# Kernel optimization log

Hardware: AMD Instinct MI355X
Metric: run time of the kernel (lower is better)

## Reference

```python
import jax, jax.numpy as jnp
import numpy as np
from jax import lax

DN = ('NCHW', 'OIHW', 'NCHW')
EPS = 1e-5


def conv2d(x, w, b, pad):
    y = lax.conv_general_dilated(x, w, (1, 1), [(pad, pad), (pad, pad)], dimension_numbers=DN)
    return y + b[None, :, None, None]


def setup_inputs() -> dict:
    B, C, G, O, H, W = 2, 64, 64, 64, 256, 256
    key = jax.random.key(0)
    ks = jax.random.split(key, 12)
    s = 0.05
    return {
        'input': jax.random.normal(ks[0], (B, C, H, W), jnp.float32),
        'guidance': jax.random.normal(ks[1], (B, G, H, W), jnp.float32),
        # channel-wise kernel-generating network (two 3x3 convs)
        'cw_w1': jax.random.normal(ks[2], (C, C + G, 3, 3), jnp.float32) * s,
        'cw_b1': jnp.zeros((C,), jnp.float32),
        'cw_w2': jax.random.normal(ks[3], (9 * C, C, 3, 3), jnp.float32) * s,
        'cw_b2': jnp.zeros((9 * C,), jnp.float32),
        # depth-wise kernel-generating network (3x3 conv -> GAP -> 1x1 conv)
        'dw_w1': jax.random.normal(ks[4], (C, C + G, 3, 3), jnp.float32) * s,
        'dw_b1': jnp.zeros((C,), jnp.float32),
        'dw_w2': jax.random.normal(ks[5], (C * O, C, 1, 1), jnp.float32) * s,
        'dw_b2': jnp.zeros((C * O,), jnp.float32),
        # BatchNorm affine params
        'bn_gamma': jnp.ones((O,), jnp.float32),
        'bn_beta': jnp.zeros((O,), jnp.float32),
    }


def reference(input, guidance, cw_w1, cw_b1, cw_w2, cw_b2,
              dw_w1, dw_b1, dw_w2, dw_b2, bn_gamma, bn_beta):
    B, C, H, W = input.shape
    kgn_in = jnp.concatenate((input, guidance), axis=1)

    # channel-wise per-pixel 3x3 weights: [B, 9C, H, W]
    cw = conv2d(jax.nn.relu(conv2d(kgn_in, cw_w1, cw_b1, 1)), cw_w2, cw_b2, 1)

    # depth-wise per-sample 1x1 weights: [B, C*O, 1, 1]
    h = jax.nn.relu(conv2d(kgn_in, dw_w1, dw_b1, 1))
    h = jnp.mean(h, axis=(2, 3), keepdims=True)  # AdaptiveAvgPool2d((1,1))
    dw = conv2d(h, dw_w2, dw_b2, 0)
    O = dw.shape[1] // C

    # guided separable conv: spatially-varying depthwise 3x3 then per-sample 1x1
    # patches ordered (C, kh, kw) channel-major -> [B, C, 9, H, W]
    patches = lax.conv_general_dilated_patches(
        input, filter_shape=(3, 3), window_strides=(1, 1), padding='SAME',
        dimension_numbers=DN).reshape(B, C, 9, H, W)
    cw = cw.reshape(B, C, 9, H, W)
    y = jnp.sum(patches * cw, axis=2)  # [B, C, H, W]

    dw = dw.reshape(B, O, C)
    z = jnp.einsum('bchw,boc->bohw', y, dw)  # per-sample 1x1 conv

    # BatchNorm2d (training-mode batch stats) + ReLU
    mu = jnp.mean(z, axis=(0, 2, 3), keepdims=True)
    var = jnp.var(z, axis=(0, 2, 3), keepdims=True)
    zn = (z - mu) * lax.rsqrt(var + EPS)
    out = jax.nn.relu(zn * bn_gamma[None, :, None, None] + bn_beta[None, :, None, None])
    return out
```

## Files before the change

kernel.cpp:

```cpp
#include <hip/hip_runtime.h>

typedef short v8s __attribute__((ext_vector_type(8)));
typedef float v4f __attribute__((ext_vector_type(4)));

__device__ inline unsigned short f2bf(float f) {
    unsigned u = __float_as_uint(f);
    u += 0x7fff + ((u >> 16) & 1);
    return (unsigned short)(u >> 16);
}
__device__ inline float bf2f(unsigned short h) {
    return __uint_as_float(((unsigned)h) << 16);
}

__device__ inline void gload_lds16(const void* g, void* l) {
    __builtin_amdgcn_global_load_lds(
        (const __attribute__((address_space(1))) unsigned*)(unsigned long long)(uintptr_t)g,
        (__attribute__((address_space(3))) unsigned*)(unsigned)(uintptr_t)l, 16, 0, 0);
}

__global__ void transpose_kernel(const float* __restrict__ input, const float* __restrict__ guidance,
                                 char* __restrict__ X0, char* __restrict__ inN)
{
    __shared__ unsigned lds[64 * 66];
    const int tid = threadIdx.x;
    const int b = blockIdx.y;
    const size_t hw0 = (size_t)blockIdx.x * 64;

    for (int it = 0; it < 16; ++it) {
        int p  = it * 4 + (tid >> 6);
        int px = tid & 63;
        size_t hw = hw0 + px;
        int c0 = 2 * p;
        float f0 = (c0 < 64) ? input[((size_t)(b * 64 + c0) << 16) + hw]
                             : guidance[((size_t)(b * 64 + c0 - 64) << 16) + hw];
        float f1 = (c0 + 1 < 64) ? input[((size_t)(b * 64 + c0 + 1) << 16) + hw]
                                 : guidance[((size_t)(b * 64 + c0 - 63) << 16) + hw];
        lds[px * 66 + p] = (unsigned)f2bf(f0) | ((unsigned)f2bf(f1) << 16);
    }
    __syncthreads();

    char* xbase = X0 + (((size_t)b * 65536 + hw0) << 8);
    for (int it = 0; it < 4; ++it) {
        int chunk = it * 256 + tid;
        int px  = chunk >> 4;
        int ofs = (chunk & 15) << 4;
        int u   = (ofs - ((px & 7) << 4)) & 255;
        const unsigned* s = &lds[px * 66 + (u >> 2)];
        *(uint4*)(xbase + px * 256 + ofs) = make_uint4(s[0], s[1], s[2], s[3]);
    }
    char* ibase = inN + (((size_t)b * 65536 + hw0) << 7);
    for (int it = 0; it < 2; ++it) {
        int chunk = it * 256 + tid;
        int px  = chunk >> 3;
        int ofs = (chunk & 7) << 4;
        int u   = (ofs - ((px & 7) << 4)) & 127;
        const unsigned* s = &lds[px * 66 + (u >> 2)];
        *(uint4*)(ibase + px * 128 + ofs) = make_uint4(s[0], s[1], s[2], s[3]);
    }
}

__global__ void prepack_all(const float* __restrict__ cw_w2, const float* __restrict__ cw_w1,
                            const float* __restrict__ dw_w1, char* __restrict__ Bp2,
                            char* __restrict__ Bp1, char* __restrict__ Bpdw)
{
    int bid = blockIdx.x;
    if (bid < 1296) {
        int t = bid * 256 + threadIdx.x;
        int jj = t & 7, lane = (t >> 3) & 63;
        int r2 = t >> 9;
        int ng = r2 % 36, r3 = r2 / 36;
        int ick = r3 & 1, tau = r3 >> 1;
        if (tau >= 9) return;
        int n  = ng * 16 + (lane & 15);
        int ic = ick * 32 + (lane >> 4) * 8 + jj;
        int oc = (n & 63) * 9 + (n >> 6);
        float v = cw_w2[(((size_t)oc * 64 + ic) * 3 + tau / 3) * 3 + tau % 3];
        *(unsigned short*)(Bp2 + (size_t)t * 2) = f2bf(v);
    } else {
        int s = bid - 1296;
        int set = (s >= 288);
        const float* src = set ? dw_w1 : cw_w1;
        char* dst = set ? Bpdw : Bp1;
        int t = (set ? s - 288 : s) * 256 + threadIdx.x;
        int jj = t & 7, lane = (t >> 3) & 63;
        int r2 = t >> 9;
        int ng = r2 & 3, r3 = r2 >> 2;
        int ick = r3 & 3, tau = r3 >> 2;
        if (tau >= 9) return;
        int n  = ng * 16 + (lane & 15);
        int ic = ick * 32 + (lane >> 4) * 8 + jj;
        float v = src[(((size_t)n * 128 + ic) * 3 + tau / 3) * 3 + tau % 3];
        *(unsigned short*)(dst + (size_t)t * 2) = f2bf(v);
    }
}

__global__ __launch_bounds__(256, 3) void conv1_mfma(
    const char* __restrict__ X0, const char* __restrict__ Bp1, const char* __restrict__ Bp2,
    const float* __restrict__ b1, const float* __restrict__ b2,
    char* __restrict__ t1, float* __restrict__ hsum)
{
    constexpr int PP = 66 * 256;
    __shared__ __align__(16) char As[3 * PP];

    const int tid = threadIdx.x, lane = tid & 63, w = tid >> 6;
    const int m16 = lane & 15, q = lane >> 4;
    const int col0 = blockIdx.x * 64;
    const int row  = blockIdx.y;
    const int b    = blockIdx.z;

    const char* rowbase = X0 + ((size_t)b * 65536) * 256;
    for (int idx = tid; idx < 3 * 1056; idx += 256) {
        int plane = idx / 1056;
        int gr = row + plane - 1;
        if ((unsigned)gr < 256u) {
            int wb  = (idx - plane * 1056) * 16;
            int pxo = wb >> 8;
            int gpx = min(max(col0 - 1 + pxo, 0), 255);
            gload_lds16(rowbase + (((size_t)gr * 256 + gpx) << 8) + (wb & 255),
                        As + (idx & ~63) * 16);
        }
    }
    __syncthreads();
    if (col0 == 0 && tid < 48)
        *(uint4*)(As + (tid / 16) * PP + (tid & 15) * 16) = make_uint4(0, 0, 0, 0);
    if (col0 == 192 && tid < 48)
        *(uint4*)(As + (tid / 16) * PP + 65 * 256 + (tid & 15) * 16) = make_uint4(0, 0, 0, 0);
    __syncthreads();

    v4f acc[4][2];
#pragma unroll
    for (int mg = 0; mg < 4; ++mg) { acc[mg][0] = (v4f)(0.f); acc[mg][1] = (v4f)(0.f); }

    const int boff = (w << 10) + (lane << 4);
    for (int ty = 0; ty < 3; ++ty) {
        int gr = row + ty - 1;
        if ((unsigned)gr >= 256u) continue;
        const char* plane = As + ty * PP;
        for (int tx = 0; tx < 3; ++tx) {
#pragma unroll
            for (int ick = 0; ick < 4; ++ick) {
                const int kstep = (ty * 3 + tx) * 4 + ick;
                v8s af[4];
#pragma unroll
                for (int mg = 0; mg < 4; ++mg) {
                    int px  = col0 + mg * 16 + m16 + tx - 1;
                    int tpx = mg * 16 + m16 + tx;
                    int off = (ick * 64 + q * 16 + ((px & 7) << 4)) & 255;
                    af[mg] = *(const v8s*)(plane + tpx * 256 + off);
                }
                v8s bf0 = *(const v8s*)(Bp1 + (size_t)kstep * 4096 + boff);
                v8s bf1 = *(const v8s*)(Bp2 + (size_t)kstep * 4096 + boff);
#pragma unroll
                for (int mg = 0; mg < 4; ++mg)
                    acc[mg][0] = __builtin_amdgcn_mfma_f32_16x16x32_bf16(af[mg], bf0, acc[mg][0], 0, 0, 0);
#pragma unroll
                for (int mg = 0; mg < 4; ++mg)
                    acc[mg][1] = __builtin_amdgcn_mfma_f32_16x16x32_bf16(af[mg], bf1, acc[mg][1], 0, 0, 0);
            }
        }
    }

    const int oc = w * 16 + m16;
    {
        float bb = b1[oc];
        char* dst = t1 + (((size_t)(b * 256 + row)) << 8) * 128;
#pragma unroll
        for (int mg = 0; mg < 4; ++mg)
#pragma unroll
            for (int r = 0; r < 4; ++r) {
                int px = col0 + mg * 16 + (q << 2) + r;
                float v = fmaxf(acc[mg][0][r] + bb, 0.f);
                *(unsigned short*)(dst + (size_t)px * 128 + ((oc * 2 + ((px & 7) << 4)) & 127)) = f2bf(v);
            }
    }
    {
        float bb = b2[oc];
        float s = 0.f;
#pragma unroll
        for (int mg = 0; mg < 4; ++mg)
#pragma unroll
            for (int r = 0; r < 4; ++r) s += fmaxf(acc[mg][1][r] + bb, 0.f);
        s += __shfl_xor(s, 16, 64);
        s += __shfl_xor(s, 32, 64);
        if (lane < 16) atomicAdd(&hsum[b * 64 + oc], s);
    }
}

__global__ void dwfused_kernel(const float* __restrict__ hsum, const float* __restrict__ w2,
                               const float* __restrict__ b2, char* __restrict__ dwp)
{
    __shared__ float h[64];
    int t = blockIdx.x * 256 + threadIdx.x;
    int b = t >> 12;
    if (threadIdx.x < 64) h[threadIdx.x] = hsum[b * 64 + threadIdx.x] * (1.f / 65536.f);
    __syncthreads();
    int jj = t & 7, lane = (t >> 3) & 63;
    int r = t >> 9;
    int owg = r & 3, kick = (r >> 2) & 1;
    int o = owg * 16 + (lane & 15);
    int c = kick * 32 + ((lane >> 4) << 3) + jj;
    int n = o * 64 + c;
    float a = 0.f;
#pragma unroll
    for (int k = 0; k < 64; ++k) a = fmaf(h[k], w2[(size_t)n * 64 + k], a);
    *(unsigned short*)(dwp + (size_t)t * 2) = f2bf(a + b2[n]);
}

__global__ __launch_bounds__(256, 2) void conv2yz_kernel(
    const char* __restrict__ t1, const char* __restrict__ inN,
    const char* __restrict__ Bp2, const char* __restrict__ dwp,
    const float* __restrict__ cw_b2, float* __restrict__ zout)
{
    constexpr int PPA = 66 * 128;
    __shared__ __align__(16) char As[3 * PPA];
    __shared__ __align__(16) char Pt[3 * PPA];
    __shared__ __align__(16) char Ys[8192];
    __shared__ __align__(16) char Dw[8192];

    const int tid = threadIdx.x, lane = tid & 63, w = tid >> 6;
    const int m16 = lane & 15, q = lane >> 4;
    const int col0 = blockIdx.x * 64;
    const int row  = blockIdx.y;
    const int b    = blockIdx.z;
    const int c_lane = w * 16 + m16;

    for (int idx = tid; idx < 512; idx += 256)
        gload_lds16(dwp + (size_t)b * 8192 + idx * 16, Dw + (idx & ~63) * 16);
    const char* arow = t1  + ((size_t)b * 65536) * 128;
    const char* prow = inN + ((size_t)b * 65536) * 128;
    for (int idx = tid; idx < 3 * 528; idx += 256) {
        int plane = idx / 528;
        int gr = row + plane - 1;
        if ((unsigned)gr < 256u) {
            int wb  = (idx - plane * 528) * 16;
            int pxo = wb >> 7;
            int gpx = min(max(col0 - 1 + pxo, 0), 255);
            size_t goff = (((size_t)gr * 256 + gpx) << 7) + (wb & 127);
            gload_lds16(arow + goff, As + (idx & ~63) * 16);
            gload_lds16(prow + goff, Pt + (idx & ~63) * 16);
        }
    }
    __syncthreads();
    if (col0 == 0 && tid < 24) {
        *(uint4*)(As + (tid / 8) * PPA + (tid & 7) * 16) = make_uint4(0, 0, 0, 0);
        *(uint4*)(Pt + (tid / 8) * PPA + (tid & 7) * 16) = make_uint4(0, 0, 0, 0);
    }
    if (col0 == 192 && tid < 24) {
        *(uint4*)(As + (tid / 8) * PPA + 65 * 128 + (tid & 7) * 16) = make_uint4(0, 0, 0, 0);
        *(uint4*)(Pt + (tid / 8) * PPA + 65 * 128 + (tid & 7) * 16) = make_uint4(0, 0, 0, 0);
    }
    __syncthreads();

    float bias9[9];
#pragma unroll
    for (int j = 0; j < 9; ++j) bias9[j] = cw_b2[c_lane * 9 + j];

    v4f acc[4][9];
#pragma unroll
    for (int mg = 0; mg < 4; ++mg)
#pragma unroll
        for (int ng = 0; ng < 9; ++ng) acc[mg][ng] = (v4f)(0.f);

    const int boff = (w << 10) + (lane << 4);
    for (int ty = 0; ty < 3; ++ty) {
        int gr = row + ty - 1;
        if ((unsigned)gr >= 256u) continue;
        const char* plane = As + ty * PPA;
#pragma unroll 1
        for (int tx = 0; tx < 3; ++tx) {
#pragma unroll
            for (int ick = 0; ick < 2; ++ick) {
                const int kstep = (ty * 3 + tx) * 2 + ick;
                v8s af[4];
#pragma unroll
                for (int mg = 0; mg < 4; ++mg) {
                    int px  = col0 + mg * 16 + m16 + tx - 1;
                    int tpx = mg * 16 + m16 + tx;
                    int off = (ick * 64 + q * 16 + ((px & 7) << 4)) & 127;
                    af[mg] = *(const v8s*)(plane + tpx * 128 + off);
                }
                const char* bbase = Bp2 + (size_t)kstep * 36864 + boff;
#pragma unroll
                for (int ng = 0; ng < 9; ++ng) {
                    v8s bf = *(const v8s*)(bbase + (ng << 12));
#pragma unroll
                    for (int mg = 0; mg < 4; ++mg)
                        acc[mg][ng] = __builtin_amdgcn_mfma_f32_16x16x32_bf16(af[mg], bf, acc[mg][ng], 0, 0, 0);
                }
            }
        }
    }

    float yv[4][4];
#pragma unroll
    for (int mg = 0; mg < 4; ++mg)
#pragma unroll
        for (int r = 0; r < 4; ++r) yv[mg][r] = 0.f;

    for (int jy = 0; jy < 3; ++jy) {
        if ((unsigned)(row + jy - 1) >= 256u) continue;
        const char* pp = Pt + jy * PPA;
        for (int jx = 0; jx < 3; ++jx) {
            const int j = jy * 3 + jx;
            const float bj = bias9[j];
#pragma unroll
            for (int mg = 0; mg < 4; ++mg)
#pragma unroll
                for (int r = 0; r < 4; ++r) {
                    int tpx = mg * 16 + (q << 2) + r + jx;
                    unsigned short pv = *(const unsigned short*)
                        (pp + tpx * 128 + ((c_lane * 2 + (((tpx - 1) & 7) << 4)) & 127));
                    yv[mg][r] = fmaf(acc[mg][j][r] + bj, bf2f(pv), yv[mg][r]);
                }
        }
    }

#pragma unroll
    for (int mg = 0; mg < 4; ++mg)
#pragma unroll
        for (int r = 0; r < 4; ++r) {
            int px_t = mg * 16 + (q << 2) + r;
            *(unsigned short*)(Ys + px_t * 128 + ((c_lane * 2 + ((px_t & 7) << 4)) & 127)) = f2bf(yv[mg][r]);
        }
    __syncthreads();

    v4f zacc[4];
#pragma unroll
    for (int mg = 0; mg < 4; ++mg) zacc[mg] = (v4f)(0.f);
#pragma unroll
    for (int kick = 0; kick < 2; ++kick) {
        v8s bf = *(const v8s*)(Dw + (((kick << 2) + w) << 10) + (lane << 4));
#pragma unroll
        for (int mg2 = 0; mg2 < 4; ++mg2) {
            int off = ((kick << 6) + (q << 4) + ((m16 & 7) << 4)) & 127;
            v8s af2 = *(const v8s*)(Ys + (mg2 * 16 + m16) * 128 + off);
            zacc[mg2] = __builtin_amdgcn_mfma_f32_16x16x32_bf16(af2, bf, zacc[mg2], 0, 0, 0);
        }
    }

    const int o = w * 16 + m16;
    float* zp = zout + (((size_t)(b * 64 + o)) << 16) + ((size_t)row << 8);
#pragma unroll
    for (int mg2 = 0; mg2 < 4; ++mg2) {
        float4 vv = make_float4(zacc[mg2][0], zacc[mg2][1], zacc[mg2][2], zacc[mg2][3]);
        *(float4*)(zp + col0 + mg2 * 16 + (q << 2)) = vv;
    }
}

__global__ void stats_kernel(const float* __restrict__ z, float* __restrict__ s1, float* __restrict__ s2)
{
    int o = blockIdx.x, ch = blockIdx.y;
    float a1 = 0.f, a2 = 0.f;
    for (int t = threadIdx.x; t < 8192; t += 256) {
        float v0 = z[((size_t)o << 16) + (ch << 13) + t];
        float v1 = z[((size_t)(64 + o) << 16) + (ch << 13) + t];
        a1 += v0 + v1;
        a2 += v0 * v0 + v1 * v1;
    }
#pragma unroll
    for (int d = 32; d > 0; d >>= 1) { a1 += __shfl_xor(a1, d, 64); a2 += __shfl_xor(a2, d, 64); }
    __shared__ float r1[4], r2[4];
    int w = threadIdx.x >> 6;
    if ((threadIdx.x & 63) == 0) { r1[w] = a1; r2[w] = a2; }
    __syncthreads();
    if (threadIdx.x == 0) {
        atomicAdd(&s1[o], r1[0] + r1[1] + r1[2] + r1[3]);
        atomicAdd(&s2[o], r2[0] + r2[1] + r2[2] + r2[3]);
    }
}

__global__ void bn_kernel(const float* __restrict__ z, const float* __restrict__ s1,
                          const float* __restrict__ s2, const float* __restrict__ gamma,
                          const float* __restrict__ beta, float* __restrict__ outp)
{
    size_t idx = ((size_t)blockIdx.x * 256 + threadIdx.x) * 4;
    int o = (int)((idx >> 16) & 63);
    float mu  = s1[o] * (1.f / 131072.f);
    float var = s2[o] * (1.f / 131072.f) - mu * mu;
    float rs  = rsqrtf(var + 1e-5f);
    float scale = gamma[o] * rs;
    float shift = beta[o] - mu * scale;
    float4 v = *(const float4*)(z + idx);
    v.x = fmaxf(v.x * scale + shift, 0.f);
    v.y = fmaxf(v.y * scale + shift, 0.f);
    v.z = fmaxf(v.z * scale + shift, 0.f);
    v.w = fmaxf(v.w * scale + shift, 0.f);
    *(float4*)(outp + idx) = v;
}

extern "C" void kernel_launch(void* const* d_in, const int* in_sizes, int n_in,
                              void* d_out, int out_size, void* d_ws, size_t ws_size,
                              hipStream_t stream)
{
    const float* input    = (const float*)d_in[0];
    const float* guidance = (const float*)d_in[1];
    const float* cw_w1    = (const float*)d_in[2];
    const float* cw_b1    = (const float*)d_in[3];
    const float* cw_w2    = (const float*)d_in[4];
    const float* cw_b2    = (const float*)d_in[5];
    const float* dw_w1    = (const float*)d_in[6];
    const float* dw_b1    = (const float*)d_in[7];
    const float* dw_w2    = (const float*)d_in[8];
    const float* dw_b2    = (const float*)d_in[9];
    const float* gamma    = (const float*)d_in[10];
    const float* beta     = (const float*)d_in[11];

    char* ws = (char*)d_ws;
    char*  inN   = ws;
    char*  t1    = ws + 16777216;
    char*  Bp1   = ws + 33554432;
    char*  Bpdw  = ws + 33701888;
    char*  Bp2   = ws + 33849344;
    float* hsum  = (float*)(ws + 34512896);
    float* s1    = (float*)(ws + 34513408);
    float* s2    = (float*)(ws + 34513664);
    char*  dwp   = ws + 34513920;

    char* X0 = (char*)d_out;

    hipMemsetAsync(hsum, 0, 1024, stream);

    transpose_kernel<<<dim3(1024, 2), 256, 0, stream>>>(input, guidance, X0, inN);
    prepack_all<<<1872, 256, 0, stream>>>(cw_w2, cw_w1, dw_w1, Bp2, Bp1, Bpdw);

    conv1_mfma<<<dim3(4, 256, 2), 256, 0, stream>>>(X0, Bp1, Bpdw, cw_b1, dw_b1, t1, hsum);
    dwfused_kernel<<<32, 256, 0, stream>>>(hsum, dw_w2, dw_b2, dwp);

    conv2yz_kernel<<<dim3(4, 256, 2), 256, 0, stream>>>(t1, inN, Bp2, dwp, cw_b2, (float*)d_out);

    stats_kernel<<<dim3(64, 8), 256, 0, stream>>>((const float*)d_out, s1, s2);
    bn_kernel<<<8192, 256, 0, stream>>>((const float*)d_out, s1, s2, gamma, beta, (float*)d_out);
}
```

Measured before the change: 324.3 us.

## Compute two rows per conv1 block and fuse BN statistics into conv2 epilogue

conv1 now handles two output rows per block. It stages four input row planes in LDS and reuses each loaded A fragment and weight fragment for both rows, halving the grid and cutting redundant LDS fills and weight loads. This raises LDS use and lowers occupancy from 3 to 2 blocks per CU. The conv2 kernel now loads all nine weight fragments ahead of the MFMAs and changes which loops are unrolled. It also accumulates per-channel sum and sum-of-squares in its epilogue with atomics, which removes the separate stats kernel and its full re-read of z, at the cost of more atomics and register pressure.

```diff
diff --git a/kernel.cpp b/kernel.cpp
--- a/kernel.cpp
+++ b/kernel.cpp
@@ -94,24 +94,24 @@
     }
 }
 
-__global__ __launch_bounds__(256, 3) void conv1_mfma(
+__global__ __launch_bounds__(256, 2) void conv1_mfma(
     const char* __restrict__ X0, const char* __restrict__ Bp1, const char* __restrict__ Bp2,
     const float* __restrict__ b1, const float* __restrict__ b2,
     char* __restrict__ t1, float* __restrict__ hsum)
 {
     constexpr int PP = 66 * 256;
-    __shared__ __align__(16) char As[3 * PP];
+    __shared__ __align__(16) char As[4 * PP];
 
     const int tid = threadIdx.x, lane = tid & 63, w = tid >> 6;
     const int m16 = lane & 15, q = lane >> 4;
     const int col0 = blockIdx.x * 64;
-    const int row  = blockIdx.y;
+    const int row0 = blockIdx.y * 2;
     const int b    = blockIdx.z;
 
     const char* rowbase = X0 + ((size_t)b * 65536) * 256;
-    for (int idx = tid; idx < 3 * 1056; idx += 256) {
+    for (int idx = tid; idx < 4 * 1056; idx += 256) {
         int plane = idx / 1056;
-        int gr = row + plane - 1;
+        int gr = row0 + plane - 1;
         if ((unsigned)gr < 256u) {
             int wb  = (idx - plane * 1056) * 16;
             int pxo = wb >> 8;
@@ -121,25 +121,35 @@
         }
     }
     __syncthreads();
-    if (col0 == 0 && tid < 48)
-        *(uint4*)(As + (tid / 16) * PP + (tid & 15) * 16) = make_uint4(0, 0, 0, 0);
-    if (col0 == 192 && tid < 48)
-        *(uint4*)(As + (tid / 16) * PP + 65 * 256 + (tid & 15) * 16) = make_uint4(0, 0, 0, 0);
-    __syncthreads();
-
-    v4f acc[4][2];
-#pragma unroll
-    for (int mg = 0; mg < 4; ++mg) { acc[mg][0] = (v4f)(0.f); acc[mg][1] = (v4f)(0.f); }
+    if (col0 == 0 && tid < 64)
+        *(uint4*)(As + (tid >> 4) * PP + (tid & 15) * 16) = make_uint4(0, 0, 0, 0);
+    if (col0 == 192 && tid < 64)
+        *(uint4*)(As + (tid >> 4) * PP + 65 * 256 + (tid & 15) * 16) = make_uint4(0, 0, 0, 0);
+    __syncthreads();
+
+    v4f acc[2][4][2];
+#pragma unroll
+    for (int rr = 0; rr < 2; ++rr)
+#pragma unroll
+        for (int mg = 0; mg < 4; ++mg) { acc[rr][mg][0] = (v4f)(0.f); acc[rr][mg][1] = (v4f)(0.f); }
 
     const int boff = (w << 10) + (lane << 4);
-    for (int ty = 0; ty < 3; ++ty) {
-        int gr = row + ty - 1;
-        if ((unsigned)gr >= 256u) continue;
-        const char* plane = As + ty * PP;
-        for (int tx = 0; tx < 3; ++tx) {
-#pragma unroll
-            for (int ick = 0; ick < 4; ++ick) {
-                const int kstep = (ty * 3 + tx) * 4 + ick;
+#pragma unroll
+    for (int tx = 0; tx < 3; ++tx) {
+#pragma unroll
+        for (int ick = 0; ick < 4; ++ick) {
+            v8s b0p, b1p;
+#pragma unroll
+            for (int p = 0; p < 4; ++p) {
+                v8s b0c, b1c;
+                if (p <= 2) {
+                    const int kstep = (p * 3 + tx) * 4 + ick;
+                    b0c = *(const v8s*)(Bp1 + (size_t)kstep * 4096 + boff);
+                    b1c = *(const v8s*)(Bp2 + (size_t)kstep * 4096 + boff);
+                }
+                const int grp = row0 + p - 1;
+                const bool pv = (unsigned)grp < 256u;
+                const char* plane = As + p * PP;
                 v8s af[4];
 #pragma unroll
                 for (int mg = 0; mg < 4; ++mg) {
@@ -148,41 +158,52 @@
                     int off = (ick * 64 + q * 16 + ((px & 7) << 4)) & 255;
                     af[mg] = *(const v8s*)(plane + tpx * 256 + off);
                 }
-                v8s bf0 = *(const v8s*)(Bp1 + (size_t)kstep * 4096 + boff);
-                v8s bf1 = *(const v8s*)(Bp2 + (size_t)kstep * 4096 + boff);
-#pragma unroll
-                for (int mg = 0; mg < 4; ++mg)
-                    acc[mg][0] = __builtin_amdgcn_mfma_f32_16x16x32_bf16(af[mg], bf0, acc[mg][0], 0, 0, 0);
-#pragma unroll
-                for (int mg = 0; mg < 4; ++mg)
-                    acc[mg][1] = __builtin_amdgcn_mfma_f32_16x16x32_bf16(af[mg], bf1, acc[mg][1], 0, 0, 0);
+                if (pv && p <= 2) {
+#pragma unroll
+                    for (int mg = 0; mg < 4; ++mg) {
+                        acc[0][mg][0] = __builtin_amdgcn_mfma_f32_16x16x32_bf16(af[mg], b0c, acc[0][mg][0], 0, 0, 0);
+                        acc[0][mg][1] = __builtin_amdgcn_mfma_f32_16x16x32_bf16(af[mg], b1c, acc[0][mg][1], 0, 0, 0);
+                    }
+                }
+                if (pv && p >= 1) {
+#pragma unroll
+                    for (int mg = 0; mg < 4; ++mg) {
+                        acc[1][mg][0] = __builtin_amdgcn_mfma_f32_16x16x32_bf16(af[mg], b0p, acc[1][mg][0], 0, 0, 0);
+                        acc[1][mg][1] = __builtin_amdgcn_mfma_f32_16x16x32_bf16(af[mg], b1p, acc[1][mg][1], 0, 0, 0);
+                    }
+                }
+                b0p = b0c; b1p = b1c;
             }
         }
     }
 
     const int oc = w * 16 + m16;
-    {
-        float bb = b1[oc];
-        char* dst = t1 + (((size_t)(b * 256 + row)) << 8) * 128;
-#pragma unroll
-        for (int mg = 0; mg < 4; ++mg)
-#pragma unroll
-            for (int r = 0; r < 4; ++r) {
-                int px = col0 + mg * 16 + (q << 2) + r;
-                float v = fmaxf(acc[mg][0][r] + bb, 0.f);
-                *(unsigned short*)(dst + (size_t)px * 128 + ((oc * 2 + ((px & 7) << 4)) & 127)) = f2bf(v);
-            }
-    }
-    {
-        float bb = b2[oc];
-        float s = 0.f;
-#pragma unroll
-        for (int mg = 0; mg < 4; ++mg)
-#pragma unroll
-            for (int r = 0; r < 4; ++r) s += fmaxf(acc[mg][1][r] + bb, 0.f);
-        s += __shfl_xor(s, 16, 64);
-        s += __shfl_xor(s, 32, 64);
-        if (lane < 16) atomicAdd(&hsum[b * 64 + oc], s);
+#pragma unroll
+    for (int rr = 0; rr < 2; ++rr) {
+        const int row = row0 + rr;
+        {
+            float bb = b1[oc];
+            char* dst = t1 + (((size_t)(b * 256 + row)) << 8) * 128;
+#pragma unroll
+            for (int mg = 0; mg < 4; ++mg)
+#pragma unroll
+                for (int r = 0; r < 4; ++r) {
+                    int px = col0 + mg * 16 + (q << 2) + r;
+                    float v = fmaxf(acc[rr][mg][0][r] + bb, 0.f);
+                    *(unsigned short*)(dst + (size_t)px * 128 + ((oc * 2 + ((px & 7) << 4)) & 127)) = f2bf(v);
+                }
+        }
+        {
+            float bb = b2[oc];
+            float s = 0.f;
+#pragma unroll
+            for (int mg = 0; mg < 4; ++mg)
+#pragma unroll
+                for (int r = 0; r < 4; ++r) s += fmaxf(acc[rr][mg][1][r] + bb, 0.f);
+            s += __shfl_xor(s, 16, 64);
+            s += __shfl_xor(s, 32, 64);
+            if (lane < 16) atomicAdd(&hsum[b * 64 + oc], s);
+        }
     }
 }
 
@@ -209,7 +230,8 @@
 __global__ __launch_bounds__(256, 2) void conv2yz_kernel(
     const char* __restrict__ t1, const char* __restrict__ inN,
     const char* __restrict__ Bp2, const char* __restrict__ dwp,
-    const float* __restrict__ cw_b2, float* __restrict__ zout)
+    const float* __restrict__ cw_b2, float* __restrict__ zout,
+    float* __restrict__ s1g, float* __restrict__ s2g)
 {
     constexpr int PPA = 66 * 128;
     __shared__ __align__(16) char As[3 * PPA];
@@ -262,15 +284,20 @@
         for (int ng = 0; ng < 9; ++ng) acc[mg][ng] = (v4f)(0.f);
 
     const int boff = (w << 10) + (lane << 4);
+#pragma unroll 1
     for (int ty = 0; ty < 3; ++ty) {
         int gr = row + ty - 1;
         if ((unsigned)gr >= 256u) continue;
         const char* plane = As + ty * PPA;
-#pragma unroll 1
+#pragma unroll
         for (int tx = 0; tx < 3; ++tx) {
 #pragma unroll
             for (int ick = 0; ick < 2; ++ick) {
                 const int kstep = (ty * 3 + tx) * 2 + ick;
+                const char* bbase = Bp2 + (size_t)kstep * 36864 + boff;
+                v8s bf[9];
+#pragma unroll
+                for (int ng = 0; ng < 9; ++ng) bf[ng] = *(const v8s*)(bbase + (ng << 12));
                 v8s af[4];
 #pragma unroll
                 for (int mg = 0; mg < 4; ++mg) {
@@ -279,14 +306,11 @@
                     int off = (ick * 64 + q * 16 + ((px & 7) << 4)) & 127;
                     af[mg] = *(const v8s*)(plane + tpx * 128 + off);
                 }
-                const char* bbase = Bp2 + (size_t)kstep * 36864 + boff;
-#pragma unroll
-                for (int ng = 0; ng < 9; ++ng) {
-                    v8s bf = *(const v8s*)(bbase + (ng << 12));
+#pragma unroll
+                for (int ng = 0; ng < 9; ++ng)
 #pragma unroll
                     for (int mg = 0; mg < 4; ++mg)
-                        acc[mg][ng] = __builtin_amdgcn_mfma_f32_16x16x32_bf16(af[mg], bf, acc[mg][ng], 0, 0, 0);
-                }
+                        acc[mg][ng] = __builtin_amdgcn_mfma_f32_16x16x32_bf16(af[mg], bf[ng], acc[mg][ng], 0, 0, 0);
             }
         }
     }
@@ -340,33 +364,17 @@
 
     const int o = w * 16 + m16;
     float* zp = zout + (((size_t)(b * 64 + o)) << 16) + ((size_t)row << 8);
+    float a1 = 0.f, a2 = 0.f;
 #pragma unroll
     for (int mg2 = 0; mg2 < 4; ++mg2) {
         float4 vv = make_float4(zacc[mg2][0], zacc[mg2][1], zacc[mg2][2], zacc[mg2][3]);
+        a1 += vv.x + vv.y + vv.z + vv.w;
+        a2 += vv.x * vv.x + vv.y * vv.y + vv.z * vv.z + vv.w * vv.w;
         *(float4*)(zp + col0 + mg2 * 16 + (q << 2)) = vv;
     }
-}
-
-__global__ void stats_kernel(const float* __restrict__ z, float* __restrict__ s1, float* __restrict__ s2)
-{
-    int o = blockIdx.x, ch = blockIdx.y;
-    float a1 = 0.f, a2 = 0.f;
-    for (int t = threadIdx.x; t < 8192; t += 256) {
-        float v0 = z[((size_t)o << 16) + (ch << 13) + t];
-        float v1 = z[((size_t)(64 + o) << 16) + (ch << 13) + t];
-        a1 += v0 + v1;
-        a2 += v0 * v0 + v1 * v1;
-    }
-#pragma unroll
-    for (int d = 32; d > 0; d >>= 1) { a1 += __shfl_xor(a1, d, 64); a2 += __shfl_xor(a2, d, 64); }
-    __shared__ float r1[4], r2[4];
-    int w = threadIdx.x >> 6;
-    if ((threadIdx.x & 63) == 0) { r1[w] = a1; r2[w] = a2; }
-    __syncthreads();
-    if (threadIdx.x == 0) {
-        atomicAdd(&s1[o], r1[0] + r1[1] + r1[2] + r1[3]);
-        atomicAdd(&s2[o], r2[0] + r2[1] + r2[2] + r2[3]);
-    }
+    a1 += __shfl_xor(a1, 16, 64); a1 += __shfl_xor(a1, 32, 64);
+    a2 += __shfl_xor(a2, 16, 64); a2 += __shfl_xor(a2, 32, 64);
+    if (lane < 16) { atomicAdd(&s1g[o], a1); atomicAdd(&s2g[o], a2); }
 }
 
 __global__ void bn_kernel(const float* __restrict__ z, const float* __restrict__ s1,
@@ -423,11 +431,11 @@
     transpose_kernel<<<dim3(1024, 2), 256, 0, stream>>>(input, guidance, X0, inN);
     prepack_all<<<1872, 256, 0, stream>>>(cw_w2, cw_w1, dw_w1, Bp2, Bp1, Bpdw);
 
-    conv1_mfma<<<dim3(4, 256, 2), 256, 0, stream>>>(X0, Bp1, Bpdw, cw_b1, dw_b1, t1, hsum);
+    conv1_mfma<<<dim3(4, 128, 2), 256, 0, stream>>>(X0, Bp1, Bpdw, cw_b1, dw_b1, t1, hsum);
     dwfused_kernel<<<32, 256, 0, stream>>>(hsum, dw_w2, dw_b2, dwp);
 
-    conv2yz_kernel<<<dim3(4, 256, 2), 256, 0, stream>>>(t1, inN, Bp2, dwp, cw_b2, (float*)d_out);
-
-    stats_kernel<<<dim3(64, 8), 256, 0, stream>>>((const float*)d_out, s1, s2);
+    conv2yz_kernel<<<dim3(4, 256, 2), 256, 0, stream>>>(t1, inN, Bp2, dwp, cw_b2,
+                                                        (float*)d_out, s1, s2);
+
     bn_kernel<<<8192, 256, 0, stream>>>((const float*)d_out, s1, s2, gamma, beta, (float*)d_out);
 }
```

Result: slower. 331.0 us (+2.1%).
